# Optimization experiments

Measured on AMD Instinct MI355X. Metric: run time of the kernel, lower is better.

The kernel has to match this reference:

```python
import jax, jax.numpy as jnp
import numpy as np

B, C, P, N = 16, 512, 4, 1024


def setup_inputs() -> dict:
    key = jax.random.key(0)
    k1, k2, k3, k4, k5 = jax.random.split(key, 5)
    s = 1.0 / np.sqrt(C)
    return {
        "x": jax.random.normal(k1, (B, C, P, N), dtype=jnp.float32),
        "w_qkv": jax.random.normal(k2, (1 + 2 * C, C), dtype=jnp.float32) * s,
        "b_qkv": jax.random.normal(k3, (1 + 2 * C,), dtype=jnp.float32) * 0.01,
        "w_out": jax.random.normal(k4, (C, C), dtype=jnp.float32) * s,
        "b_out": jax.random.normal(k5, (C,), dtype=jnp.float32) * 0.01,
    }


def reference(x, w_qkv, b_qkv, w_out, b_out):
    # 1x1 conv == channel GEMM: [B,C,P,N] x [O,C] -> [B,O,P,N]
    qkv = jnp.einsum('bcpn,oc->bopn', x, w_qkv) + b_qkv[None, :, None, None]
    query = qkv[:, :1]            # [B,1,P,N]
    key_t = qkv[:, 1:1 + C]       # [B,C,P,N]
    value = qkv[:, 1 + C:]        # [B,C,P,N]
    # softmax over token axis N (attn_drop is identity at inference)
    context_scores = jax.nn.softmax(query, axis=-1)           # [B,1,P,N]
    # broadcast mul + reduce over N (fused; no explicit expand)
    context_vector = jnp.sum(key_t * context_scores, axis=-1, keepdims=True)  # [B,C,P,1]
    out = jax.nn.relu(value) * context_vector                 # [B,C,P,N]
    out = jnp.einsum('bcpn,oc->bopn', out, w_out) + b_out[None, :, None, None]
    return out
```

## Files before the change

kernel.cpp:

```cpp
#include <hip/hip_runtime.h>
#include <math.h>

#define BB 16
#define C  512
#define P  4
#define NN 1024
#define BP (BB*P)
#define PN (P*NN)

typedef short bf16x8 __attribute__((ext_vector_type(8)));
typedef float f32x4  __attribute__((ext_vector_type(4)));
typedef unsigned short ushort_t;

__device__ __forceinline__ ushort_t bf16rne(float f) {
    unsigned u = __float_as_uint(f);
    u += 0x7FFFu + ((u >> 16) & 1u);
    return (ushort_t)(u >> 16);
}
__device__ __forceinline__ float bf16tof(ushort_t h) {
    return __uint_as_float(((unsigned)h) << 16);
}

__global__ __launch_bounds__(256) void k_split(const float* __restrict__ w_qkv,
                                               const float* __restrict__ w_out,
                                               ushort_t* __restrict__ wv_hi,
                                               ushort_t* __restrict__ wv_lo,
                                               ushort_t* __restrict__ wo_hi,
                                               ushort_t* __restrict__ wo_lo) {
    const int i = blockIdx.x * 256 + threadIdx.x;
    const int e = i * 4;
    const float* src; ushort_t *dh, *dl; int off;
    if (e < C * C) { src = w_qkv + (size_t)(1 + C) * C; dh = wv_hi; dl = wv_lo; off = e; }
    else           { src = w_out;                       dh = wo_hi; dl = wo_lo; off = e - C * C; }
    const float4 v = *reinterpret_cast<const float4*>(src + off);
    const float vv[4] = {v.x, v.y, v.z, v.w};
    ushort_t h[4], l[4];
    #pragma unroll
    for (int j = 0; j < 4; ++j) {
        h[j] = bf16rne(vv[j]);
        l[j] = bf16rne(vv[j] - bf16tof(h[j]));
    }
    uint2 ph, pl;
    ph.x = (unsigned)h[0] | ((unsigned)h[1] << 16);
    ph.y = (unsigned)h[2] | ((unsigned)h[3] << 16);
    pl.x = (unsigned)l[0] | ((unsigned)l[1] << 16);
    pl.y = (unsigned)l[2] | ((unsigned)l[3] << 16);
    *reinterpret_cast<uint2*>(dh + off) = ph;
    *reinterpret_cast<uint2*>(dl + off) = pl;
}

__global__ __launch_bounds__(256) void k_query(const float* __restrict__ x,
                                               const float* __restrict__ w_qkv,
                                               float4* __restrict__ qpart4) {
    __shared__ float wq[64];
    const int bp = blockIdx.x >> 3, cc = blockIdx.x & 7;
    const int b = bp >> 2, p = bp & 3;
    const int tid = threadIdx.x;
    if (tid < 64) wq[tid] = w_qkv[cc * 64 + tid];
    __syncthreads();
    const float* xb = x + (size_t)b * C * PN + (size_t)p * NN;
    f32x4 acc[8];
    #pragma unroll
    for (int a = 0; a < 8; ++a) acc[a] = (f32x4){0.f, 0.f, 0.f, 0.f};
    #pragma unroll 8
    for (int i = 0; i < 64; ++i) {
        const float4 v = *reinterpret_cast<const float4*>(xb + (size_t)(cc * 64 + i) * PN + tid * 4);
        const float wv = wq[i];
        acc[i & 7][0] = fmaf(v.x, wv, acc[i & 7][0]);
        acc[i & 7][1] = fmaf(v.y, wv, acc[i & 7][1]);
        acc[i & 7][2] = fmaf(v.z, wv, acc[i & 7][2]);
        acc[i & 7][3] = fmaf(v.w, wv, acc[i & 7][3]);
    }
    f32x4 s = ((acc[0] + acc[1]) + (acc[2] + acc[3])) + ((acc[4] + acc[5]) + (acc[6] + acc[7]));
    float4 o; o.x = s[0]; o.y = s[1]; o.z = s[2]; o.w = s[3];
    qpart4[(cc * BP + bp) * 256 + tid] = o;
}

__global__ __launch_bounds__(256) void k_softmax(const float4* __restrict__ qpart4,
                                                 float4* __restrict__ scores4) {
    __shared__ float red[256];
    const int bp = blockIdx.x, tid = threadIdx.x;
    float v[4] = {0.f, 0.f, 0.f, 0.f};
    #pragma unroll
    for (int cc = 0; cc < 8; ++cc) {
        const float4 q = qpart4[(cc * BP + bp) * 256 + tid];
        v[0] += q.x; v[1] += q.y; v[2] += q.z; v[3] += q.w;
    }
    float m = fmaxf(fmaxf(v[0], v[1]), fmaxf(v[2], v[3]));
    red[tid] = m; __syncthreads();
    for (int s = 128; s > 0; s >>= 1) {
        if (tid < s) red[tid] = fmaxf(red[tid], red[tid + s]);
        __syncthreads();
    }
    m = red[0]; __syncthreads();
    float sum = 0.f;
    #pragma unroll
    for (int j = 0; j < 4; ++j) { v[j] = expf(v[j] - m); sum += v[j]; }
    red[tid] = sum; __syncthreads();
    for (int s = 128; s > 0; s >>= 1) {
        if (tid < s) red[tid] += red[tid + s];
        __syncthreads();
    }
    const float inv = 1.0f / red[0];
    float4 o; o.x = v[0] * inv; o.y = v[1] * inv; o.z = v[2] * inv; o.w = v[3] * inv;
    scores4[bp * 256 + tid] = o;
}

__global__ __launch_bounds__(256) void k_xs(const float* __restrict__ x,
                                            const float4* __restrict__ scores4,
                                            float* __restrict__ xs) {
    __shared__ float4 sc4[256];
    const int bp = blockIdx.x >> 4, cc = blockIdx.x & 15;
    const int b = bp >> 2, p = bp & 3;
    const int tid = threadIdx.x;
    sc4[tid] = scores4[bp * 256 + tid];
    __syncthreads();
    const int wave = tid >> 6, lane = tid & 63;
    const float* xb = x + (size_t)b * C * PN + (size_t)p * NN;
    #pragma unroll
    for (int r = 0; r < 8; ++r) {
        const int c = cc * 32 + wave * 8 + r;
        const float4* row4 = reinterpret_cast<const float4*>(xb + (size_t)c * PN);
        float a0 = 0.f, a1 = 0.f, a2 = 0.f, a3 = 0.f;
        #pragma unroll
        for (int j = 0; j < 4; ++j) {
            const float4 xv = row4[lane + 64 * j];
            const float4 sv = sc4[lane + 64 * j];
            a0 = fmaf(xv.x, sv.x, a0);
            a1 = fmaf(xv.y, sv.y, a1);
            a2 = fmaf(xv.z, sv.z, a2);
            a3 = fmaf(xv.w, sv.w, a3);
        }
        float acc = (a0 + a1) + (a2 + a3);
        #pragma unroll
        for (int off = 32; off > 0; off >>= 1) acc += __shfl_down(acc, off);
        if (lane == 0) xs[bp * C + c] = acc;
    }
}

__global__ __launch_bounds__(256) void k_cv(const float* __restrict__ xs,
                                            const float* __restrict__ w_qkv,
                                            const float* __restrict__ b_qkv,
                                            float* __restrict__ cv) {
    __shared__ float xsl[C];
    const int bp = blockIdx.x, tid = threadIdx.x;
    for (int i = tid; i < C; i += 256) xsl[i] = xs[bp * C + i];
    __syncthreads();
    const int wave = tid >> 6, lane = tid & 63;
    for (int o = wave; o < C; o += 4) {
        const float* wr = w_qkv + (size_t)(1 + o) * C;
        float acc = 0.f;
        #pragma unroll
        for (int j = 0; j < 8; ++j) acc = fmaf(wr[lane + 64 * j], xsl[lane + 64 * j], acc);
        #pragma unroll
        for (int off = 32; off > 0; off >>= 1) acc += __shfl_down(acc, off);
        if (lane == 0) cv[bp * C + o] = acc + b_qkv[1 + o];
    }
}

#define XTFH 2048

__global__ __launch_bounds__(512, 1) void k_vo(
    const float* __restrict__ x,
    const ushort_t* __restrict__ wv_hi, const ushort_t* __restrict__ wv_lo,
    const ushort_t* __restrict__ wo_hi, const ushort_t* __restrict__ wo_lo,
    const float* __restrict__ b_qkv, const float* __restrict__ b_out,
    const float* __restrict__ cv, float* __restrict__ out) {

    extern __shared__ char lds_raw[];
    ushort_t* actf_hi = (ushort_t*)lds_raw;
    ushort_t* actf_lo = actf_hi + 16 * 4 * 64 * 8;
    ushort_t* xtf     = actf_lo + 16 * 4 * 64 * 8;

    const int nt = blockIdx.x, bp = blockIdx.y;
    const int b = bp >> 2, p = bp & 3;
    const int n0 = nt * 64;
    const int tid = threadIdx.x;
    const int w  = tid >> 6;
    const int l  = tid & 63;
    const int lr = l & 15;
    const int lg = l >> 4;

    const float* xb = x + (size_t)b * C * PN + (size_t)p * NN + n0;

    const int g_col = tid & 63;
    const int g_k4  = (tid >> 6) * 4;
    const int st_off = (((g_col >> 4) * 64 + (g_k4 >> 3) * 16 + (g_col & 15)) * 8) + (g_k4 & 7);

    f32x4 acc[4][4];
    #pragma unroll
    for (int m = 0; m < 4; ++m)
        #pragma unroll
        for (int n = 0; n < 4; ++n) acc[m][n] = (f32x4){0.f, 0.f, 0.f, 0.f};

    {
        float xg[4];
        #pragma unroll
        for (int jj = 0; jj < 4; ++jj) xg[jj] = xb[(size_t)(g_k4 + jj) * PN + g_col];
        ushort_t h[4], lo[4];
        #pragma unroll
        for (int jj = 0; jj < 4; ++jj) {
            h[jj]  = bf16rne(xg[jj]);
            lo[jj] = bf16rne(xg[jj] - bf16tof(h[jj]));
        }
        uint2 ph, pl;
        ph.x = (unsigned)h[0]  | ((unsigned)h[1]  << 16);
        ph.y = (unsigned)h[2]  | ((unsigned)h[3]  << 16);
        pl.x = (unsigned)lo[0] | ((unsigned)lo[1] << 16);
        pl.y = (unsigned)lo[2] | ((unsigned)lo[3] << 16);
        *reinterpret_cast<uint2*>(&xtf[st_off])        = ph;
        *reinterpret_cast<uint2*>(&xtf[XTFH + st_off]) = pl;
    }
    __syncthreads();

    for (int kt = 0; kt < 16; ++kt) {
        const int cur = kt & 1;
        float xg[4];
        if (kt < 15) {
            #pragma unroll
            for (int jj = 0; jj < 4; ++jj)
                xg[jj] = xb[(size_t)((kt + 1) * 32 + g_k4 + jj) * PN + g_col];
        }
        const ushort_t* xh = xtf + cur * 2 * XTFH;
        const ushort_t* xl = xh + XTFH;
        bf16x8 bh[4], bl[4];
        #pragma unroll
        for (int n = 0; n < 4; ++n) {
            bh[n] = *reinterpret_cast<const bf16x8*>(&xh[(n * 64 + l) * 8]);
            bl[n] = *reinterpret_cast<const bf16x8*>(&xl[(n * 64 + l) * 8]);
        }
        #pragma unroll
        for (int m = 0; m < 4; ++m) {
            const int row = w * 64 + m * 16 + lr;
            const bf16x8 ah = *reinterpret_cast<const bf16x8*>(&wv_hi[(size_t)row * C + kt * 32 + lg * 8]);
            const bf16x8 al = *reinterpret_cast<const bf16x8*>(&wv_lo[(size_t)row * C + kt * 32 + lg * 8]);
            #pragma unroll
            for (int n = 0; n < 4; ++n) {
                acc[m][n] = __builtin_amdgcn_mfma_f32_16x16x32_bf16(ah, bh[n], acc[m][n], 0, 0, 0);
                acc[m][n] = __builtin_amdgcn_mfma_f32_16x16x32_bf16(ah, bl[n], acc[m][n], 0, 0, 0);
                acc[m][n] = __builtin_amdgcn_mfma_f32_16x16x32_bf16(al, bh[n], acc[m][n], 0, 0, 0);
            }
        }
        if (kt < 15) {
            ushort_t* dh = xtf + (cur ^ 1) * 2 * XTFH;
            ushort_t h[4], lo[4];
            #pragma unroll
            for (int jj = 0; jj < 4; ++jj) {
                h[jj]  = bf16rne(xg[jj]);
                lo[jj] = bf16rne(xg[jj] - bf16tof(h[jj]));
            }
            uint2 ph, pl;
            ph.x = (unsigned)h[0]  | ((unsigned)h[1]  << 16);
            ph.y = (unsigned)h[2]  | ((unsigned)h[3]  << 16);
            pl.x = (unsigned)lo[0] | ((unsigned)lo[1] << 16);
            pl.y = (unsigned)lo[2] | ((unsigned)lo[3] << 16);
            *reinterpret_cast<uint2*>(&dh[st_off])        = ph;
            *reinterpret_cast<uint2*>(&dh[XTFH + st_off]) = pl;
        }
        __syncthreads();
    }

    {
        const float* bq  = b_qkv + 1 + C;
        const float* cvb = cv + bp * C;
        #pragma unroll
        for (int m = 0; m < 4; ++m) {
            const int rbase = w * 64 + m * 16 + lg * 4;
            const int ktp = w * 2 + (m >> 1);
            const int lgp = (m * 2 + (lg >> 1)) & 3;
            const int j0p = (lg & 1) * 4;
            float bias[4], cvv[4];
            #pragma unroll
            for (int j = 0; j < 4; ++j) { bias[j] = bq[rbase + j]; cvv[j] = cvb[rbase + j]; }
            #pragma unroll
            for (int n = 0; n < 4; ++n) {
                ushort_t hh[4], ll[4];
                #pragma unroll
                for (int j = 0; j < 4; ++j) {
                    const float av = fmaxf(acc[m][n][j] + bias[j], 0.f) * cvv[j];
                    hh[j] = bf16rne(av);
                    ll[j] = bf16rne(av - bf16tof(hh[j]));
                }
                uint2 ph, pl;
                ph.x = (unsigned)hh[0] | ((unsigned)hh[1] << 16);
                ph.y = (unsigned)hh[2] | ((unsigned)hh[3] << 16);
                pl.x = (unsigned)ll[0] | ((unsigned)ll[1] << 16);
                pl.y = (unsigned)ll[2] | ((unsigned)ll[3] << 16);
                const int off = ((ktp * 4 + n) * 64 + lgp * 16 + lr) * 8 + j0p;
                *reinterpret_cast<uint2*>(&actf_hi[off]) = ph;
                *reinterpret_cast<uint2*>(&actf_lo[off]) = pl;
            }
        }
    }
    __syncthreads();

    f32x4 acc2[4][4];
    #pragma unroll
    for (int m = 0; m < 4; ++m)
        #pragma unroll
        for (int n = 0; n < 4; ++n) acc2[m][n] = (f32x4){0.f, 0.f, 0.f, 0.f};

    for (int kt = 0; kt < 16; ++kt) {
        bf16x8 bh[4], bl[4];
        #pragma unroll
        for (int n = 0; n < 4; ++n) {
            bh[n] = *reinterpret_cast<const bf16x8*>(&actf_hi[((kt * 4 + n) * 64 + l) * 8]);
            bl[n] = *reinterpret_cast<const bf16x8*>(&actf_lo[((kt * 4 + n) * 64 + l) * 8]);
        }
        #pragma unroll
        for (int m = 0; m < 4; ++m) {
            const int row = w * 64 + m * 16 + lr;
            const bf16x8 ah = *reinterpret_cast<const bf16x8*>(&wo_hi[(size_t)row * C + kt * 32 + lg * 8]);
            const bf16x8 al = *reinterpret_cast<const bf16x8*>(&wo_lo[(size_t)row * C + kt * 32 + lg * 8]);
            #pragma unroll
            for (int n = 0; n < 4; ++n) {
                acc2[m][n] = __builtin_amdgcn_mfma_f32_16x16x32_bf16(ah, bh[n], acc2[m][n], 0, 0, 0);
                acc2[m][n] = __builtin_amdgcn_mfma_f32_16x16x32_bf16(ah, bl[n], acc2[m][n], 0, 0, 0);
                acc2[m][n] = __builtin_amdgcn_mfma_f32_16x16x32_bf16(al, bh[n], acc2[m][n], 0, 0, 0);
            }
        }
    }

    #pragma unroll
    for (int m = 0; m < 4; ++m) {
        #pragma unroll
        for (int j = 0; j < 4; ++j) {
            const int row = w * 64 + m * 16 + lg * 4 + j;
            const float bo = b_out[row];
            float* orow = out + ((size_t)(b * C + row) * P + p) * NN + n0;
            #pragma unroll
            for (int n = 0; n < 4; ++n)
                orow[n * 16 + lr] = acc2[m][n][j] + bo;
        }
    }
}

extern "C" void kernel_launch(void* const* d_in, const int* in_sizes, int n_in,
                              void* d_out, int out_size, void* d_ws, size_t ws_size,
                              hipStream_t stream) {
    const float* x     = (const float*)d_in[0];
    const float* w_qkv = (const float*)d_in[1];
    const float* b_qkv = (const float*)d_in[2];
    const float* w_out = (const float*)d_in[3];
    const float* b_out = (const float*)d_in[4];
    float* out = (float*)d_out;

    float* qpart  = (float*)d_ws;
    float* scores = qpart + 8 * BP * NN;
    float* xs     = scores + BP * NN;
    float* cv     = xs + BP * C;
    ushort_t* wsp = (ushort_t*)(cv + BP * C);
    ushort_t* wv_hi = wsp;
    ushort_t* wv_lo = wsp + C * C;
    ushort_t* wo_hi = wsp + 2 * C * C;
    ushort_t* wo_lo = wsp + 3 * C * C;

    k_split  <<<dim3(512),     256, 0, stream>>>(w_qkv, w_out, wv_hi, wv_lo, wo_hi, wo_lo);
    k_query  <<<dim3(BP * 8),  256, 0, stream>>>(x, w_qkv, (float4*)qpart);
    k_softmax<<<dim3(BP),      256, 0, stream>>>((const float4*)qpart, (float4*)scores);
    k_xs     <<<dim3(BP * 16), 256, 0, stream>>>(x, (const float4*)scores, xs);
    k_cv     <<<dim3(BP),      256, 0, stream>>>(xs, w_qkv, b_qkv, cv);

    const size_t ldsbytes = (size_t)(2 * 16 * 4 * 64 * 8 + 2 * 2 * XTFH) * sizeof(ushort_t);
    k_vo<<<dim3(16, BP), 512, ldsbytes, stream>>>(x, wv_hi, wv_lo, wo_hi, wo_lo,
                                                  b_qkv, b_out, cv, out);
}
```

Measured before the change: 624.5 us.

## Split fused value/out GEMM into two kernels with global intermediate activations

Replaces the single fused value-projection plus output-projection kernel with two kernels. The first, k_value, writes the relu(value)*context activations as bf16 hi/lo pairs into a global workspace, already laid out as MFMA tiles. The second, k_out, reads them back for the output GEMM. This removes the large LDS activation buffer and the one-block-per-CU launch bound, so more blocks can be resident per CU. The cost is about 128 MB of extra global write-and-read traffic plus one more kernel launch. The fused kernel remains as a fallback when the workspace is too small.

```diff
diff --git a/kernel.cpp b/kernel.cpp
--- a/kernel.cpp
+++ b/kernel.cpp
@@ -11,6 +11,10 @@
 typedef short bf16x8 __attribute__((ext_vector_type(8)));
 typedef float f32x4  __attribute__((ext_vector_type(4)));
 typedef unsigned short ushort_t;
+
+#define XTFH 2048
+#define TILE_SH 32768
+#define NTILES 1024
 
 __device__ __forceinline__ ushort_t bf16rne(float f) {
     unsigned u = __float_as_uint(f);
@@ -158,9 +162,194 @@
     }
 }
 
-#define XTFH 2048
-
-__global__ __launch_bounds__(512, 1) void k_vo(
+__global__ __launch_bounds__(512) void k_value(
+    const float* __restrict__ x,
+    const ushort_t* __restrict__ wv_hi, const ushort_t* __restrict__ wv_lo,
+    const float* __restrict__ b_qkv, const float* __restrict__ cv,
+    ushort_t* __restrict__ act_hi, ushort_t* __restrict__ act_lo) {
+
+    __shared__ ushort_t xtf[2 * 2 * XTFH];
+
+    const int nt = blockIdx.x, bp = blockIdx.y;
+    const int b = bp >> 2, p = bp & 3;
+    const int n0 = nt * 64;
+    const int tid = threadIdx.x;
+    const int w  = tid >> 6;
+    const int l  = tid & 63;
+    const int lr = l & 15;
+    const int lg = l >> 4;
+
+    const float* xb = x + (size_t)b * C * PN + (size_t)p * NN + n0;
+    const size_t tb = (size_t)(bp * 16 + nt) * TILE_SH;
+
+    const int g_col = tid & 63;
+    const int g_k4  = (tid >> 6) * 4;
+    const int st_off = (((g_col >> 4) * 64 + (g_k4 >> 3) * 16 + (g_col & 15)) * 8) + (g_k4 & 7);
+
+    f32x4 acc[4][4];
+    #pragma unroll
+    for (int m = 0; m < 4; ++m)
+        #pragma unroll
+        for (int n = 0; n < 4; ++n) acc[m][n] = (f32x4){0.f, 0.f, 0.f, 0.f};
+
+    {
+        float xg[4];
+        #pragma unroll
+        for (int jj = 0; jj < 4; ++jj) xg[jj] = xb[(size_t)(g_k4 + jj) * PN + g_col];
+        ushort_t h[4], lo[4];
+        #pragma unroll
+        for (int jj = 0; jj < 4; ++jj) {
+            h[jj]  = bf16rne(xg[jj]);
+            lo[jj] = bf16rne(xg[jj] - bf16tof(h[jj]));
+        }
+        uint2 ph, pl;
+        ph.x = (unsigned)h[0]  | ((unsigned)h[1]  << 16);
+        ph.y = (unsigned)h[2]  | ((unsigned)h[3]  << 16);
+        pl.x = (unsigned)lo[0] | ((unsigned)lo[1] << 16);
+        pl.y = (unsigned)lo[2] | ((unsigned)lo[3] << 16);
+        *reinterpret_cast<uint2*>(&xtf[st_off])        = ph;
+        *reinterpret_cast<uint2*>(&xtf[XTFH + st_off]) = pl;
+    }
+    __syncthreads();
+
+    for (int kt = 0; kt < 16; ++kt) {
+        const int cur = kt & 1;
+        float xg[4];
+        if (kt < 15) {
+            #pragma unroll
+            for (int jj = 0; jj < 4; ++jj)
+                xg[jj] = xb[(size_t)((kt + 1) * 32 + g_k4 + jj) * PN + g_col];
+        }
+        const ushort_t* xh = xtf + cur * 2 * XTFH;
+        const ushort_t* xl = xh + XTFH;
+        bf16x8 bh[4], bl[4];
+        #pragma unroll
+        for (int n = 0; n < 4; ++n) {
+            bh[n] = *reinterpret_cast<const bf16x8*>(&xh[(n * 64 + l) * 8]);
+            bl[n] = *reinterpret_cast<const bf16x8*>(&xl[(n * 64 + l) * 8]);
+        }
+        #pragma unroll
+        for (int m = 0; m < 4; ++m) {
+            const int row = w * 64 + m * 16 + lr;
+            const bf16x8 ah = *reinterpret_cast<const bf16x8*>(&wv_hi[(size_t)row * C + kt * 32 + lg * 8]);
+            const bf16x8 al = *reinterpret_cast<const bf16x8*>(&wv_lo[(size_t)row * C + kt * 32 + lg * 8]);
+            #pragma unroll
+            for (int n = 0; n < 4; ++n) {
+                acc[m][n] = __builtin_amdgcn_mfma_f32_16x16x32_bf16(ah, bh[n], acc[m][n], 0, 0, 0);
+                acc[m][n] = __builtin_amdgcn_mfma_f32_16x16x32_bf16(ah, bl[n], acc[m][n], 0, 0, 0);
+                acc[m][n] = __builtin_amdgcn_mfma_f32_16x16x32_bf16(al, bh[n], acc[m][n], 0, 0, 0);
+            }
+        }
+        if (kt < 15) {
+            ushort_t* dh = xtf + (cur ^ 1) * 2 * XTFH;
+            ushort_t h[4], lo[4];
+            #pragma unroll
+            for (int jj = 0; jj < 4; ++jj) {
+                h[jj]  = bf16rne(xg[jj]);
+                lo[jj] = bf16rne(xg[jj] - bf16tof(h[jj]));
+            }
+            uint2 ph, pl;
+            ph.x = (unsigned)h[0]  | ((unsigned)h[1]  << 16);
+            ph.y = (unsigned)h[2]  | ((unsigned)h[3]  << 16);
+            pl.x = (unsigned)lo[0] | ((unsigned)lo[1] << 16);
+            pl.y = (unsigned)lo[2] | ((unsigned)lo[3] << 16);
+            *reinterpret_cast<uint2*>(&dh[st_off])        = ph;
+            *reinterpret_cast<uint2*>(&dh[XTFH + st_off]) = pl;
+        }
+        __syncthreads();
+    }
+
+    {
+        const float* bq  = b_qkv + 1 + C;
+        const float* cvb = cv + bp * C;
+        #pragma unroll
+        for (int m = 0; m < 4; ++m) {
+            const int rbase = w * 64 + m * 16 + lg * 4;
+            const int ktp = w * 2 + (m >> 1);
+            const int lgp = (m * 2 + (lg >> 1)) & 3;
+            const int j0p = (lg & 1) * 4;
+            float bias[4], cvv[4];
+            #pragma unroll
+            for (int j = 0; j < 4; ++j) { bias[j] = bq[rbase + j]; cvv[j] = cvb[rbase + j]; }
+            #pragma unroll
+            for (int n = 0; n < 4; ++n) {
+                ushort_t hh[4], ll[4];
+                #pragma unroll
+                for (int j = 0; j < 4; ++j) {
+                    const float av = fmaxf(acc[m][n][j] + bias[j], 0.f) * cvv[j];
+                    hh[j] = bf16rne(av);
+                    ll[j] = bf16rne(av - bf16tof(hh[j]));
+                }
+                uint2 ph, pl;
+                ph.x = (unsigned)hh[0] | ((unsigned)hh[1] << 16);
+                ph.y = (unsigned)hh[2] | ((unsigned)hh[3] << 16);
+                pl.x = (unsigned)ll[0] | ((unsigned)ll[1] << 16);
+                pl.y = (unsigned)ll[2] | ((unsigned)ll[3] << 16);
+                const size_t off = tb + ((ktp * 4 + n) * 64 + lgp * 16 + lr) * 8 + j0p;
+                *reinterpret_cast<uint2*>(&act_hi[off]) = ph;
+                *reinterpret_cast<uint2*>(&act_lo[off]) = pl;
+            }
+        }
+    }
+}
+
+__global__ __launch_bounds__(512) void k_out(
+    const ushort_t* __restrict__ act_hi, const ushort_t* __restrict__ act_lo,
+    const ushort_t* __restrict__ wo_hi, const ushort_t* __restrict__ wo_lo,
+    const float* __restrict__ b_out, float* __restrict__ out) {
+
+    const int nt = blockIdx.x, bp = blockIdx.y;
+    const int b = bp >> 2, p = bp & 3;
+    const int n0 = nt * 64;
+    const int tid = threadIdx.x;
+    const int w  = tid >> 6;
+    const int l  = tid & 63;
+    const int lr = l & 15;
+    const int lg = l >> 4;
+    const size_t tb = (size_t)(bp * 16 + nt) * TILE_SH;
+
+    f32x4 acc2[4][4];
+    #pragma unroll
+    for (int m = 0; m < 4; ++m)
+        #pragma unroll
+        for (int n = 0; n < 4; ++n) acc2[m][n] = (f32x4){0.f, 0.f, 0.f, 0.f};
+
+    for (int kt = 0; kt < 16; ++kt) {
+        bf16x8 bh[4], bl[4];
+        #pragma unroll
+        for (int n = 0; n < 4; ++n) {
+            bh[n] = *reinterpret_cast<const bf16x8*>(&act_hi[tb + ((kt * 4 + n) * 64 + l) * 8]);
+            bl[n] = *reinterpret_cast<const bf16x8*>(&act_lo[tb + ((kt * 4 + n) * 64 + l) * 8]);
+        }
+        #pragma unroll
+        for (int m = 0; m < 4; ++m) {
+            const int row = w * 64 + m * 16 + lr;
+            const bf16x8 ah = *reinterpret_cast<const bf16x8*>(&wo_hi[(size_t)row * C + kt * 32 + lg * 8]);
+            const bf16x8 al = *reinterpret_cast<const bf16x8*>(&wo_lo[(size_t)row * C + kt * 32 + lg * 8]);
+            #pragma unroll
+            for (int n = 0; n < 4; ++n) {
+                acc2[m][n] = __builtin_amdgcn_mfma_f32_16x16x32_bf16(ah, bh[n], acc2[m][n], 0, 0, 0);
+                acc2[m][n] = __builtin_amdgcn_mfma_f32_16x16x32_bf16(ah, bl[n], acc2[m][n], 0, 0, 0);
+                acc2[m][n] = __builtin_amdgcn_mfma_f32_16x16x32_bf16(al, bh[n], acc2[m][n], 0, 0, 0);
+            }
+        }
+    }
+
+    #pragma unroll
+    for (int m = 0; m < 4; ++m) {
+        #pragma unroll
+        for (int j = 0; j < 4; ++j) {
+            const int row = w * 64 + m * 16 + lg * 4 + j;
+            const float bo = b_out[row];
+            float* orow = out + ((size_t)(b * C + row) * P + p) * NN + n0;
+            #pragma unroll
+            for (int n = 0; n < 4; ++n)
+                orow[n * 16 + lr] = acc2[m][n][j] + bo;
+        }
+    }
+}
+
+__global__ __launch_bounds__(512, 1) void k_vo_fused(
     const float* __restrict__ x,
     const ushort_t* __restrict__ wv_hi, const ushort_t* __restrict__ wv_lo,
     const ushort_t* __restrict__ wo_hi, const ushort_t* __restrict__ wo_lo,
@@ -354,6 +543,9 @@
     ushort_t* wv_lo = wsp + C * C;
     ushort_t* wo_hi = wsp + 2 * C * C;
     ushort_t* wo_lo = wsp + 3 * C * C;
+    ushort_t* act_hi = wsp + 4 * (size_t)C * C;
+    ushort_t* act_lo = act_hi + (size_t)NTILES * TILE_SH;
+    const size_t need = (size_t)((char*)(act_lo + (size_t)NTILES * TILE_SH) - (char*)d_ws);
 
     k_split  <<<dim3(512),     256, 0, stream>>>(w_qkv, w_out, wv_hi, wv_lo, wo_hi, wo_lo);
     k_query  <<<dim3(BP * 8),  256, 0, stream>>>(x, w_qkv, (float4*)qpart);
@@ -361,7 +553,12 @@
     k_xs     <<<dim3(BP * 16), 256, 0, stream>>>(x, (const float4*)scores, xs);
     k_cv     <<<dim3(BP),      256, 0, stream>>>(xs, w_qkv, b_qkv, cv);
 
-    const size_t ldsbytes = (size_t)(2 * 16 * 4 * 64 * 8 + 2 * 2 * XTFH) * sizeof(ushort_t);
-    k_vo<<<dim3(16, BP), 512, ldsbytes, stream>>>(x, wv_hi, wv_lo, wo_hi, wo_lo,
-                                                  b_qkv, b_out, cv, out);
-}
+    if (ws_size >= need) {
+        k_value<<<dim3(16, BP), 512, 0, stream>>>(x, wv_hi, wv_lo, b_qkv, cv, act_hi, act_lo);
+        k_out  <<<dim3(16, BP), 512, 0, stream>>>(act_hi, act_lo, wo_hi, wo_lo, b_out, out);
+    } else {
+        const size_t ldsbytes = (size_t)(2 * 16 * 4 * 64 * 8 + 2 * 2 * XTFH) * sizeof(ushort_t);
+        k_vo_fused<<<dim3(16, BP), 512, ldsbytes, stream>>>(x, wv_hi, wv_lo, wo_hi, wo_lo,
+                                                            b_qkv, b_out, cv, out);
+    }
+}
```

Result: slower. 659.8 us (+5.7%).
